# Optimization experiments

Measured on AMD Instinct MI355X. Metric: run time of the kernel, lower is better.

## Reference

```python
import jax, jax.numpy as jnp
import numpy as np

B, N, C = 8, 1025, 768  # batch, tokens (1 CLS + 32*32 patches), channels
H = 12                  # heads
D = C // H              # head dim = 64
EPS = 1e-6

def _rot(x):
    # stack([-x[..., 1::2], x[..., ::2]], -1).reshape(x.shape)
    return jnp.stack([-x[..., 1::2], x[..., ::2]], axis=-1).reshape(x.shape)

def apply_rot_embed_cat(x, emb):
    # emb: [N-1, 2*D] = concat(sin, cos); x: [B, H, N-1, D]
    sin, cos = jnp.split(emb, 2, axis=-1)
    return x * cos + _rot(x) * sin

def setup_inputs() -> dict:
    key = jax.random.key(0)
    ks = jax.random.split(key, 8)
    s = 0.02
    return {
        "x": jax.random.normal(ks[0], (B, N, C), jnp.float32),
        "rope": jax.random.normal(ks[1], (N - 1, 2 * D), jnp.float32),
        "w_qkv": jax.random.normal(ks[2], (C, 3 * C), jnp.float32) * s,
        "q_bias": jax.random.normal(ks[3], (C,), jnp.float32) * s,
        "v_bias": jax.random.normal(ks[4], (C,), jnp.float32) * s,
        "gamma": jnp.ones((C,), jnp.float32),
        "beta": jnp.zeros((C,), jnp.float32),
        "w_proj": jax.random.normal(ks[5], (C, C), jnp.float32) * s,
        "b_proj": jnp.zeros((C,), jnp.float32),
    }

def reference(x, rope, w_qkv, q_bias, v_bias, gamma, beta, w_proj, b_proj):
    scale = D ** (-0.5)
    qkv_bias = jnp.concatenate([q_bias, jnp.zeros_like(q_bias), v_bias], axis=0)
    qkv = x @ w_qkv + qkv_bias  # [B, N, 3C]
    qkv = qkv.reshape(B, N, 3, H, D).transpose(2, 0, 3, 1, 4)  # [3, B, H, N, D]
    q, k, v = qkv[0], qkv[1], qkv[2]
    # RoPE on non-CLS tokens only
    q = jnp.concatenate([q[:, :, :1], apply_rot_embed_cat(q[:, :, 1:], rope)], axis=2)
    k = jnp.concatenate([k[:, :, :1], apply_rot_embed_cat(k[:, :, 1:], rope)], axis=2)
    attn = jnp.einsum('bhqd,bhkd->bhqk', q * scale, k)
    attn = jax.nn.softmax(attn, axis=-1)
    y = jnp.einsum('bhqk,bhkd->bhqd', attn, v)
    y = y.transpose(0, 2, 1, 3).reshape(B, N, C)
    # LayerNorm
    mu = jnp.mean(y, axis=-1, keepdims=True)
    var = jnp.mean(jnp.square(y - mu), axis=-1, keepdims=True)
    y = (y - mu) * jax.lax.rsqrt(var + EPS) * gamma + beta
    return y @ w_proj + b_proj
```

## Files before the change

kernel.cpp:

```cpp
#include <hip/hip_runtime.h>

typedef __bf16 bf16_t;
typedef __bf16 bf16x8 __attribute__((ext_vector_type(8)));
typedef float f32x4 __attribute__((ext_vector_type(4)));
typedef float f32x16 __attribute__((ext_vector_type(16)));
typedef unsigned short u16;
typedef unsigned int u32;

#define NTOK 1025
#define MTOT 8200
#define MPAD 8448
#define CDIM 768

__device__ __forceinline__ u16 f2bf(float f) {
  union { float f; unsigned u; } v; v.f = f;
  unsigned r = v.u + 0x7fffu + ((v.u >> 16) & 1u);
  return (u16)(r >> 16);
}
__device__ __forceinline__ float bf2f(u16 h) {
  union { unsigned u; float f; } v; v.u = ((unsigned)h) << 16; return v.f;
}
__device__ __forceinline__ u32 cvtpk(float lo, float hi) {
  u32 r; asm("v_cvt_pk_bf16_f32 %0, %1, %2" : "=v"(r) : "v"(lo), "v"(hi)); return r;
}
__device__ __forceinline__ void gld16(const void* g, void* l) {
  __builtin_amdgcn_global_load_lds(
      (const __attribute__((address_space(1))) unsigned*)g,
      (__attribute__((address_space(3))) unsigned*)l, 16, 0, 0);
}

__global__ void conv_x(const float4* __restrict__ in, u16* __restrict__ out, int n4) {
  int i = blockIdx.x * blockDim.x + threadIdx.x;
  if (i < n4) {
    float4 f = in[i];
    ushort4 o; o.x = f2bf(f.x); o.y = f2bf(f.y); o.z = f2bf(f.z); o.w = f2bf(f.w);
    *(ushort4*)&out[i * 4] = o;
  }
}

__global__ __launch_bounds__(256) void transp(const float* __restrict__ in,
                                              u16* __restrict__ out, int K, int N) {
  __shared__ float tile[32][33];
  int n0 = blockIdx.x * 32, k0 = blockIdx.y * 32;
  int tx = threadIdx.x & 31, ty = threadIdx.x >> 5;
#pragma unroll
  for (int i = 0; i < 4; ++i)
    tile[ty + i * 8][tx] = in[(k0 + ty + i * 8) * N + n0 + tx];
  __syncthreads();
#pragma unroll
  for (int i = 0; i < 4; ++i)
    out[(n0 + ty + i * 8) * K + k0 + tx] = f2bf(tile[tx][ty + i * 8]);
}

template <bool TRANS>
__device__ __forceinline__ void kloop128(const u16* __restrict__ A, const u16* __restrict__ Bt,
                                         int m0, int n0, u16* As, u16* Bs, int t,
                                         f32x4 (*acc)[4]) {
  const int K = 768;
  int lane = t & 63, wave = t >> 6;
  int ln = lane & 15, hi = lane >> 4;
  int wr = wave >> 1, wc = wave & 1;
  int swz = (ln & 7) << 4;
  int trow = t >> 3;
  int tcolb = (t & 7) * 16;
  int scol = ((tcolb ^ ((trow & 7) << 4)) >> 1);

  for (int k0 = 0; k0 < K; k0 += 64) {
#pragma unroll
    for (int c = 0; c < 4; ++c) {
      gld16(&A[(size_t)(m0 + c * 32 + trow) * K + k0 + scol], &As[c * 2048 + t * 8]);
      gld16(&Bt[(size_t)(n0 + c * 32 + trow) * K + k0 + scol], &Bs[c * 2048 + t * 8]);
    }
    asm volatile("s_waitcnt vmcnt(0)" ::: "memory");
    __builtin_amdgcn_s_barrier();
    asm volatile("" ::: "memory");
#pragma unroll
    for (int kk = 0; kk < 2; ++kk) {
      bf16x8 af[4], bfr[4];
#pragma unroll
      for (int i = 0; i < 4; ++i)
        af[i] = *(const bf16x8*)((const char*)&As[(wr * 64 + i * 16 + ln) * 64]
                                 + ((kk * 64 + hi * 16) ^ swz));
#pragma unroll
      for (int j = 0; j < 4; ++j)
        bfr[j] = *(const bf16x8*)((const char*)&Bs[(wc * 64 + j * 16 + ln) * 64]
                                  + ((kk * 64 + hi * 16) ^ swz));
      __builtin_amdgcn_s_setprio(1);
#pragma unroll
      for (int x = 0; x < 4; ++x)
#pragma unroll
        for (int y = 0; y < 4; ++y)
          acc[x][y] = TRANS
              ? __builtin_amdgcn_mfma_f32_16x16x32_bf16(bfr[x], af[y], acc[x][y], 0, 0, 0)
              : __builtin_amdgcn_mfma_f32_16x16x32_bf16(af[x], bfr[y], acc[x][y], 0, 0, 0);
      __builtin_amdgcn_s_setprio(0);
    }
    asm volatile("" ::: "memory");
    __builtin_amdgcn_s_barrier();
  }
}

__global__ __launch_bounds__(256) void qkv_gemm_t(
    const u16* __restrict__ A, const u16* __restrict__ Bt,
    const float* __restrict__ qbias, const float* __restrict__ rope,
    u16* __restrict__ q, u16* __restrict__ k) {
  const int NB = 12;
  __shared__ u16 As[8192], Bs[8192];
  int tau0 = blockIdx.x;
  int xcd = tau0 & 7, pos = tau0 >> 3;
  int tau = (xcd < 4) ? xcd * 98 + pos : 392 + (xcd - 4) * 97 + pos;
  int bx = tau % NB, by = tau / NB;
  int m0 = by * 128, n0 = bx * 128;
  int t = threadIdx.x;
  int lane = t & 63, wave = t >> 6;
  int ln = lane & 15, hi = lane >> 4;
  int wr = wave >> 1, wc = wave & 1;

  f32x4 acc[4][4] = {};
  kloop128<true>(A, Bt, m0, n0, As, Bs, t, acc);

  const float scale = 0.125f * 1.4426950408889634f;
#pragma unroll
  for (int ii = 0; ii < 4; ++ii) {
    int m = m0 + wr * 64 + ii * 16 + ln;
    if (m < MTOT) {
      int b = m / NTOK;
      int n = m - b * NTOK;
      const float* rp = rope + (size_t)(n - 1) * 128;
#pragma unroll
      for (int jj = 0; jj < 4; ++jj) {
        int c4 = n0 + wc * 64 + jj * 16 + hi * 4;
        int part = (c4 >= CDIM) ? 1 : 0;
        int cc = c4 - part * CDIM;
        int h = cc >> 6, d4 = cc & 63;
        float v0 = acc[jj][ii][0], v1 = acc[jj][ii][1];
        float v2 = acc[jj][ii][2], v3 = acc[jj][ii][3];
        if (part == 0) {
          float4 qb = *(const float4*)(qbias + cc);
          v0 += qb.x; v1 += qb.y; v2 += qb.z; v3 += qb.w;
        }
        float o0, o1, o2, o3;
        if (n > 0) {
          float4 sn = *(const float4*)(rp + d4);
          float4 cs = *(const float4*)(rp + 64 + d4);
          o0 = v0 * cs.x - v1 * sn.x;
          o1 = v1 * cs.y + v0 * sn.y;
          o2 = v2 * cs.z - v3 * sn.z;
          o3 = v3 * cs.w + v2 * sn.w;
        } else { o0 = v0; o1 = v1; o2 = v2; o3 = v3; }
        if (part == 0) { o0 *= scale; o1 *= scale; o2 *= scale; o3 *= scale; }
        uint2 w; w.x = cvtpk(o0, o1); w.y = cvtpk(o2, o3);
        u16* dst = (part ? k : q) + ((size_t)(h * MPAD + m)) * 64 + d4;
        *(uint2*)dst = w;
      }
    }
  }
}

__global__ __launch_bounds__(256) void qkv_gemm_v(
    const u16* __restrict__ A, const u16* __restrict__ Bt,
    const float* __restrict__ vbias, u16* __restrict__ vt) {
  const int NB = 6;
  __shared__ u16 As[8192], Bs[8192];
  int tau0 = blockIdx.x;
  int xcd = tau0 & 7, pos = tau0 >> 3;
  int tau = (xcd < 6) ? xcd * 49 + pos : 294 + (xcd - 6) * 48 + pos;
  int bx = tau % NB, by = tau / NB;
  int m0 = by * 128, n0 = 1536 + bx * 128;
  int t = threadIdx.x;
  int lane = t & 63, wave = t >> 6;
  int ln = lane & 15, hi = lane >> 4;
  int wr = wave >> 1, wc = wave & 1;

  f32x4 acc[4][4] = {};
  kloop128<false>(A, Bt, m0, n0, As, Bs, t, acc);

#pragma unroll
  for (int i = 0; i < 4; ++i) {
    int mrow = m0 + wr * 64 + i * 16 + hi * 4;
    if (mrow < MTOT) {
      bool full = (mrow + 3 < MTOT);
#pragma unroll
      for (int j = 0; j < 4; ++j) {
        int cv = n0 - 1536 + wc * 64 + j * 16 + ln;
        int h = cv >> 6, d = cv & 63;
        float vb = vbias[cv];
        float v0 = acc[i][j][0] + vb, v1 = acc[i][j][1] + vb;
        float v2 = acc[i][j][2] + vb, v3 = acc[i][j][3] + vb;
        u16* dst = vt + ((size_t)(h * 64 + d)) * MPAD + mrow;
        if (full) {
          uint2 w; w.x = cvtpk(v0, v1); w.y = cvtpk(v2, v3);
          *(uint2*)dst = w;
        } else {
          float vv[4] = {v0, v1, v2, v3};
#pragma unroll
          for (int r = 0; r < 4; ++r)
            if (mrow + r < MTOT) dst[r] = f2bf(vv[r]);
        }
      }
    }
  }
}

__global__ __launch_bounds__(256) void flash_attn(
    const u16* __restrict__ q, const u16* __restrict__ k,
    const u16* __restrict__ vt, u16* __restrict__ y) {
  __shared__ u16 smem[2][8192];
  int f = blockIdx.x;
  int xcd = f & 7, idx = f >> 3;
  int bh = xcd * 12 + idx / 9;
  int qt = idx - (idx / 9) * 9;
  int b = bh / 12, h = bh - b * 12;
  int t = threadIdx.x, lane = t & 63, w = t >> 6;
  int lq = lane & 31, h2 = lane >> 5;
  int q0 = qt * 128 + w * 32;
  bool active = (q0 < NTOK);
  int qrow = q0 + lq; if (qrow > NTOK - 1) qrow = NTOK - 1;

  const size_t kbase = ((size_t)h * MPAD + (size_t)b * NTOK) * 64;
  const size_t vbase = (size_t)h * 64 * MPAD + (size_t)b * NTOK;

  const u16* qp = q + kbase + (size_t)qrow * 64;
  bf16x8 qf[4];
#pragma unroll
  for (int s = 0; s < 4; ++s)
    qf[s] = *(const bf16x8*)&qp[s * 16 + h2 * 8];

  f32x16 acc[2] = {};
  float l = 0.f;

  auto stage = [&](int buf, int kt) {
    int t16 = t * 16;
#pragma unroll
    for (int j = 0; j < 4; ++j) {
      int off = j * 4096 + t16;
      int off2 = off & 8191;
      int row = off2 >> 7;
      int col = off2 & 127;
      int scol = col ^ ((row & 7) << 4);
      const u16* src = (j < 2)
          ? &k[kbase + (size_t)(kt + row) * 64 + (scol >> 1)]
          : &vt[vbase + (size_t)row * MPAD + kt + (scol >> 1)];
      gld16(src, (char*)&smem[buf][0] + off);
    }
  };

  stage(0, 0);
  asm volatile("s_waitcnt vmcnt(0)" ::: "memory");
  __syncthreads();

  for (int it = 0; it < 17; ++it) {
    int kt = it * 64;
    int cur = it & 1;
    if (it < 16) stage(cur ^ 1, kt + 64);

    if (active) {
      const char* kb = (const char*)&smem[cur][0];
      f32x16 sc[2] = {};
      __builtin_amdgcn_s_setprio(1);
#pragma unroll
      for (int c = 0; c < 2; ++c) {
        int krow = c * 32 + lq;
#pragma unroll
        for (int s = 0; s < 4; ++s) {
          int kcol = (s * 32 + h2 * 16) ^ ((lane & 7) << 4);
          bf16x8 kf = *(const bf16x8*)(kb + krow * 128 + kcol);
          sc[c] = __builtin_amdgcn_mfma_f32_32x32x16_bf16(kf, qf[s], sc[c], 0, 0, 0);
        }
      }
      __builtin_amdgcn_s_setprio(0);
      float p[2][16];
#pragma unroll
      for (int c = 0; c < 2; ++c)
#pragma unroll
        for (int r = 0; r < 16; ++r)
          p[c][r] = __builtin_amdgcn_exp2f(sc[c][r]);
      if (it == 16) {
#pragma unroll
        for (int c = 0; c < 2; ++c)
#pragma unroll
          for (int r = 0; r < 16; ++r) {
            int kk = kt + c * 32 + (r & 3) + 8 * (r >> 2) + 4 * h2;
            if (kk >= NTOK) p[c][r] = 0.f;
          }
      }
      float rs = 0.f;
#pragma unroll
      for (int c = 0; c < 2; ++c)
#pragma unroll
        for (int r = 0; r < 16; ++r) rs += p[c][r];
      l += rs;
      bf16x8 frag[4];
#pragma unroll
      for (int c = 0; c < 2; ++c) {
        u32 pk[8];
#pragma unroll
        for (int i = 0; i < 8; ++i) pk[i] = cvtpk(p[c][2 * i], p[c][2 * i + 1]);
        u32 x0 = __shfl_xor(pk[0], 32, 64), x1 = __shfl_xor(pk[1], 32, 64);
        u32 x2 = __shfl_xor(pk[2], 32, 64), x3 = __shfl_xor(pk[3], 32, 64);
        u32 x4 = __shfl_xor(pk[4], 32, 64), x5 = __shfl_xor(pk[5], 32, 64);
        u32 x6 = __shfl_xor(pk[6], 32, 64), x7 = __shfl_xor(pk[7], 32, 64);
        union { u32 u[4]; bf16x8 v; } u0, u1;
        u0.u[0] = h2 ? x2 : pk[0];  u0.u[1] = h2 ? x3 : pk[1];
        u0.u[2] = h2 ? pk[2] : x0;  u0.u[3] = h2 ? pk[3] : x1;
        u1.u[0] = h2 ? x6 : pk[4];  u1.u[1] = h2 ? x7 : pk[5];
        u1.u[2] = h2 ? pk[6] : x4;  u1.u[3] = h2 ? pk[7] : x5;
        frag[c * 2] = u0.v; frag[c * 2 + 1] = u1.v;
      }
      __builtin_amdgcn_s_setprio(1);
#pragma unroll
      for (int hf = 0; hf < 2; ++hf) {
        int vrow = hf * 32 + lq;
#pragma unroll
        for (int s = 0; s < 4; ++s) {
          int vcol = (s * 32 + h2 * 16) ^ ((lane & 7) << 4);
          bf16x8 vf = *(const bf16x8*)(kb + 8192 + vrow * 128 + vcol);
          acc[hf] = __builtin_amdgcn_mfma_f32_32x32x16_bf16(vf, frag[s], acc[hf], 0, 0, 0);
        }
      }
      __builtin_amdgcn_s_setprio(0);
    }
    asm volatile("s_waitcnt vmcnt(0)" ::: "memory");
    __syncthreads();
  }

  int row = q0 + lq;
  if (active && row < NTOK) {
    float lt = l + __shfl_xor(l, 32, 64);
    float inv = 1.f / lt;
    u16* yr = y + ((size_t)(b * NTOK + row)) * CDIM + h * 64;
#pragma unroll
    for (int hf = 0; hf < 2; ++hf)
#pragma unroll
      for (int g = 0; g < 4; ++g) {
        int d0 = hf * 32 + 8 * g + 4 * h2;
        ushort4 o;
        o.x = f2bf(acc[hf][g * 4 + 0] * inv);
        o.y = f2bf(acc[hf][g * 4 + 1] * inv);
        o.z = f2bf(acc[hf][g * 4 + 2] * inv);
        o.w = f2bf(acc[hf][g * 4 + 3] * inv);
        *(ushort4*)&yr[d0] = o;
      }
  }
}

__global__ __launch_bounds__(256) void lnorm(const u16* __restrict__ y,
                                             const float* __restrict__ gamma,
                                             const float* __restrict__ beta,
                                             u16* __restrict__ out) {
  int row = blockIdx.x;
  const u16* yr = y + (size_t)row * CDIM;
  int t = threadIdx.x;
  float v[3];
  float s = 0.f, s2 = 0.f;
#pragma unroll
  for (int i = 0; i < 3; ++i) {
    v[i] = bf2f(yr[t + 256 * i]);
    s += v[i]; s2 += v[i] * v[i];
  }
#pragma unroll
  for (int msk = 1; msk < 64; msk <<= 1) {
    s  += __shfl_xor(s, msk, 64);
    s2 += __shfl_xor(s2, msk, 64);
  }
  __shared__ float ws[8];
  int w = t >> 6, lane = t & 63;
  if (lane == 0) { ws[w] = s; ws[4 + w] = s2; }
  __syncthreads();
  s = ws[0] + ws[1] + ws[2] + ws[3];
  s2 = ws[4] + ws[5] + ws[6] + ws[7];
  float mu = s * (1.f / 768.f);
  float var = s2 * (1.f / 768.f) - mu * mu;
  float rstd = rsqrtf(var + 1e-6f);
#pragma unroll
  for (int i = 0; i < 3; ++i) {
    int c = t + 256 * i;
    out[(size_t)row * CDIM + c] = f2bf((v[i] - mu) * rstd * gamma[c] + beta[c]);
  }
}

__global__ __launch_bounds__(256) void proj_gemm(
    const u16* __restrict__ A, const u16* __restrict__ Bt,
    const float* __restrict__ bias, float* __restrict__ out) {
  const int NB = 6;
  __shared__ u16 As[8192], Bs[8192];
  int tau0 = blockIdx.x;
  int xcd = tau0 & 7, pos = tau0 >> 3;
  int tau = (xcd < 6) ? xcd * 49 + pos : 294 + (xcd - 6) * 48 + pos;
  int bx = tau % NB, by = tau / NB;
  int m0 = by * 128, n0 = bx * 128;
  int t = threadIdx.x;
  int lane = t & 63, wave = t >> 6;
  int ln = lane & 15, hi = lane >> 4;
  int wr = wave >> 1, wc = wave & 1;

  f32x4 acc[4][4] = {};
  kloop128<true>(A, Bt, m0, n0, As, Bs, t, acc);

#pragma unroll
  for (int ii = 0; ii < 4; ++ii) {
    int m = m0 + wr * 64 + ii * 16 + ln;
    if (m < MTOT) {
      float* dr = out + (size_t)m * CDIM;
#pragma unroll
      for (int jj = 0; jj < 4; ++jj) {
        int c4 = n0 + wc * 64 + jj * 16 + hi * 4;
        float4 bv = *(const float4*)(bias + c4);
        float4 o;
        o.x = acc[jj][ii][0] + bv.x;
        o.y = acc[jj][ii][1] + bv.y;
        o.z = acc[jj][ii][2] + bv.z;
        o.w = acc[jj][ii][3] + bv.w;
        *(float4*)(dr + c4) = o;
      }
    }
  }
}

extern "C" void kernel_launch(void* const* d_in, const int* in_sizes, int n_in,
                              void* d_out, int out_size, void* d_ws, size_t ws_size,
                              hipStream_t stream) {
  const float* x      = (const float*)d_in[0];
  const float* rope   = (const float*)d_in[1];
  const float* w_qkv  = (const float*)d_in[2];
  const float* q_bias = (const float*)d_in[3];
  const float* v_bias = (const float*)d_in[4];
  const float* gamma  = (const float*)d_in[5];
  const float* beta   = (const float*)d_in[6];
  const float* w_proj = (const float*)d_in[7];
  const float* b_proj = (const float*)d_in[8];
  float* out = (float*)d_out;

  char* ws = (char*)d_ws;
  u16* xb    = (u16*)(ws);
  u16* ybf   = (u16*)(ws);
  u16* wqkvt = (u16*)(ws + 12976128);
  u16* wprjt = (u16*)(ws + 16515072);
  u16* qbuf  = (u16*)(ws + 17694720);
  u16* ylb   = (u16*)(ws + 17694720);
  u16* kbuf  = (u16*)(ws + 30670848);
  u16* vtg   = (u16*)(ws + 43646976);

  conv_x<<<(1574400 + 255) / 256, 256, 0, stream>>>((const float4*)x, xb, 1574400);
  transp<<<dim3(2304 / 32, 768 / 32), 256, 0, stream>>>(w_qkv, wqkvt, 768, 2304);
  transp<<<dim3(768 / 32, 768 / 32), 256, 0, stream>>>(w_proj, wprjt, 768, 768);

  qkv_gemm_t<<<dim3(780), 256, 0, stream>>>(xb, wqkvt, q_bias, rope, qbuf, kbuf);
  qkv_gemm_v<<<dim3(390), 256, 0, stream>>>(xb, wqkvt, v_bias, vtg);
  flash_attn<<<dim3(864), 256, 0, stream>>>(qbuf, kbuf, vtg, ybf);
  lnorm<<<8200, 256, 0, stream>>>(ybf, gamma, beta, ylb);
  proj_gemm<<<dim3(390), 256, 0, stream>>>(ylb, wprjt, b_proj, out);
}
```

Measured before the change: 169.5 us.

## Drop LDS staging in flash attention, load K/V directly from global

Removes the double-buffered shared-memory staging of K and V tiles and the per-iteration barriers. Each wave now reads its K and V fragments directly from global memory (relying on L2/L1 caching across the four waves that share the same tiles), exits early when its query rows are out of range, and replaces the shuffle-and-select fragment exchange with v_permlane32_swap. This cuts LDS traffic and barrier stalls, but the four waves each issue their own global loads and no longer overlap the next tile's load with compute.

```diff
diff --git a/kernel.cpp b/kernel.cpp
--- a/kernel.cpp
+++ b/kernel.cpp
@@ -205,7 +205,6 @@
 __global__ __launch_bounds__(256) void flash_attn(
     const u16* __restrict__ q, const u16* __restrict__ k,
     const u16* __restrict__ vt, u16* __restrict__ y) {
-  __shared__ u16 smem[2][8192];
   int f = blockIdx.x;
   int xcd = f & 7, idx = f >> 3;
   int bh = xcd * 12 + idx / 9;
@@ -214,7 +213,7 @@
   int t = threadIdx.x, lane = t & 63, w = t >> 6;
   int lq = lane & 31, h2 = lane >> 5;
   int q0 = qt * 128 + w * 32;
-  bool active = (q0 < NTOK);
+  if (q0 >= NTOK) return;
   int qrow = q0 + lq; if (qrow > NTOK - 1) qrow = NTOK - 1;
 
   const size_t kbase = ((size_t)h * MPAD + (size_t)b * NTOK) * 64;
@@ -229,103 +228,72 @@
   f32x16 acc[2] = {};
   float l = 0.f;
 
-  auto stage = [&](int buf, int kt) {
-    int t16 = t * 16;
-#pragma unroll
-    for (int j = 0; j < 4; ++j) {
-      int off = j * 4096 + t16;
-      int off2 = off & 8191;
-      int row = off2 >> 7;
-      int col = off2 & 127;
-      int scol = col ^ ((row & 7) << 4);
-      const u16* src = (j < 2)
-          ? &k[kbase + (size_t)(kt + row) * 64 + (scol >> 1)]
-          : &vt[vbase + (size_t)row * MPAD + kt + (scol >> 1)];
-      gld16(src, (char*)&smem[buf][0] + off);
-    }
-  };
-
-  stage(0, 0);
-  asm volatile("s_waitcnt vmcnt(0)" ::: "memory");
-  __syncthreads();
-
   for (int it = 0; it < 17; ++it) {
     int kt = it * 64;
-    int cur = it & 1;
-    if (it < 16) stage(cur ^ 1, kt + 64);
-
-    if (active) {
-      const char* kb = (const char*)&smem[cur][0];
-      f32x16 sc[2] = {};
-      __builtin_amdgcn_s_setprio(1);
-#pragma unroll
-      for (int c = 0; c < 2; ++c) {
-        int krow = c * 32 + lq;
-#pragma unroll
-        for (int s = 0; s < 4; ++s) {
-          int kcol = (s * 32 + h2 * 16) ^ ((lane & 7) << 4);
-          bf16x8 kf = *(const bf16x8*)(kb + krow * 128 + kcol);
-          sc[c] = __builtin_amdgcn_mfma_f32_32x32x16_bf16(kf, qf[s], sc[c], 0, 0, 0);
+    f32x16 sc[2] = {};
+    __builtin_amdgcn_s_setprio(1);
+#pragma unroll
+    for (int c = 0; c < 2; ++c) {
+      const u16* kr = k + kbase + (size_t)(kt + c * 32 + lq) * 64 + h2 * 8;
+#pragma unroll
+      for (int s = 0; s < 4; ++s) {
+        bf16x8 kf = *(const bf16x8*)&kr[s * 16];
+        sc[c] = __builtin_amdgcn_mfma_f32_32x32x16_bf16(kf, qf[s], sc[c], 0, 0, 0);
+      }
+    }
+    __builtin_amdgcn_s_setprio(0);
+    float p[2][16];
+#pragma unroll
+    for (int c = 0; c < 2; ++c)
+#pragma unroll
+      for (int r = 0; r < 16; ++r)
+        p[c][r] = __builtin_amdgcn_exp2f(sc[c][r]);
+    if (it == 16) {
+#pragma unroll
+      for (int c = 0; c < 2; ++c)
+#pragma unroll
+        for (int r = 0; r < 16; ++r) {
+          int kk = kt + c * 32 + (r & 3) + 8 * (r >> 2) + 4 * h2;
+          if (kk >= NTOK) p[c][r] = 0.f;
         }
-      }
-      __builtin_amdgcn_s_setprio(0);
-      float p[2][16];
-#pragma unroll
-      for (int c = 0; c < 2; ++c)
-#pragma unroll
-        for (int r = 0; r < 16; ++r)
-          p[c][r] = __builtin_amdgcn_exp2f(sc[c][r]);
-      if (it == 16) {
-#pragma unroll
-        for (int c = 0; c < 2; ++c)
-#pragma unroll
-          for (int r = 0; r < 16; ++r) {
-            int kk = kt + c * 32 + (r & 3) + 8 * (r >> 2) + 4 * h2;
-            if (kk >= NTOK) p[c][r] = 0.f;
-          }
-      }
-      float rs = 0.f;
-#pragma unroll
-      for (int c = 0; c < 2; ++c)
-#pragma unroll
-        for (int r = 0; r < 16; ++r) rs += p[c][r];
-      l += rs;
-      bf16x8 frag[4];
-#pragma unroll
-      for (int c = 0; c < 2; ++c) {
-        u32 pk[8];
-#pragma unroll
-        for (int i = 0; i < 8; ++i) pk[i] = cvtpk(p[c][2 * i], p[c][2 * i + 1]);
-        u32 x0 = __shfl_xor(pk[0], 32, 64), x1 = __shfl_xor(pk[1], 32, 64);
-        u32 x2 = __shfl_xor(pk[2], 32, 64), x3 = __shfl_xor(pk[3], 32, 64);
-        u32 x4 = __shfl_xor(pk[4], 32, 64), x5 = __shfl_xor(pk[5], 32, 64);
-        u32 x6 = __shfl_xor(pk[6], 32, 64), x7 = __shfl_xor(pk[7], 32, 64);
-        union { u32 u[4]; bf16x8 v; } u0, u1;
-        u0.u[0] = h2 ? x2 : pk[0];  u0.u[1] = h2 ? x3 : pk[1];
-        u0.u[2] = h2 ? pk[2] : x0;  u0.u[3] = h2 ? pk[3] : x1;
-        u1.u[0] = h2 ? x6 : pk[4];  u1.u[1] = h2 ? x7 : pk[5];
-        u1.u[2] = h2 ? pk[6] : x4;  u1.u[3] = h2 ? pk[7] : x5;
-        frag[c * 2] = u0.v; frag[c * 2 + 1] = u1.v;
-      }
-      __builtin_amdgcn_s_setprio(1);
-#pragma unroll
-      for (int hf = 0; hf < 2; ++hf) {
-        int vrow = hf * 32 + lq;
-#pragma unroll
-        for (int s = 0; s < 4; ++s) {
-          int vcol = (s * 32 + h2 * 16) ^ ((lane & 7) << 4);
-          bf16x8 vf = *(const bf16x8*)(kb + 8192 + vrow * 128 + vcol);
-          acc[hf] = __builtin_amdgcn_mfma_f32_32x32x16_bf16(vf, frag[s], acc[hf], 0, 0, 0);
-        }
-      }
-      __builtin_amdgcn_s_setprio(0);
-    }
-    asm volatile("s_waitcnt vmcnt(0)" ::: "memory");
-    __syncthreads();
+    }
+    float rs = 0.f;
+#pragma unroll
+    for (int c = 0; c < 2; ++c)
+#pragma unroll
+      for (int r = 0; r < 16; ++r) rs += p[c][r];
+    l += rs;
+    bf16x8 frag[4];
+#pragma unroll
+    for (int c = 0; c < 2; ++c) {
+      u32 k0 = cvtpk(p[c][0], p[c][1]),  k1 = cvtpk(p[c][2], p[c][3]);
+      u32 k2 = cvtpk(p[c][4], p[c][5]),  k3 = cvtpk(p[c][6], p[c][7]);
+      u32 k4 = cvtpk(p[c][8], p[c][9]),  k5 = cvtpk(p[c][10], p[c][11]);
+      u32 k6 = cvtpk(p[c][12], p[c][13]), k7 = cvtpk(p[c][14], p[c][15]);
+      asm("v_permlane32_swap_b32 %0, %1" : "+v"(k0), "+v"(k2));
+      asm("v_permlane32_swap_b32 %0, %1" : "+v"(k1), "+v"(k3));
+      asm("v_permlane32_swap_b32 %0, %1" : "+v"(k4), "+v"(k6));
+      asm("v_permlane32_swap_b32 %0, %1" : "+v"(k5), "+v"(k7));
+      union { u32 u[4]; bf16x8 v; } u0, u1;
+      u0.u[0] = k0; u0.u[1] = k1; u0.u[2] = k2; u0.u[3] = k3;
+      u1.u[0] = k4; u1.u[1] = k5; u1.u[2] = k6; u1.u[3] = k7;
+      frag[c * 2] = u0.v; frag[c * 2 + 1] = u1.v;
+    }
+    __builtin_amdgcn_s_setprio(1);
+#pragma unroll
+    for (int hf = 0; hf < 2; ++hf) {
+      const u16* vr = vt + vbase + (size_t)(hf * 32 + lq) * MPAD + kt + h2 * 8;
+#pragma unroll
+      for (int s = 0; s < 4; ++s) {
+        bf16x8 vf = *(const bf16x8*)&vr[s * 16];
+        acc[hf] = __builtin_amdgcn_mfma_f32_32x32x16_bf16(vf, frag[s], acc[hf], 0, 0, 0);
+      }
+    }
+    __builtin_amdgcn_s_setprio(0);
   }
 
   int row = q0 + lq;
-  if (active && row < NTOK) {
+  if (row < NTOK) {
     float lt = l + __shfl_xor(l, 32, 64);
     float inv = 1.f / lt;
     u16* yr = y + ((size_t)(b * NTOK + row)) * CDIM + h * 64;
```

Result: slower. 386.8 us (+128.2%).
